# Optimization experiments

Hardware: AMD Instinct MI355X
Metric: run time of the kernel (lower is better)

The kernel has to match this reference:

```python
import jax, jax.numpy as jnp
import numpy as np

D_MODEL = 768
D_STATE = 16
D_CONV = 4
EXPAND = 2
HEADDIM = 64
D_INNER = EXPAND * D_MODEL          # 1536
NHEADS = D_INNER // HEADDIM         # 24
CONV_DIM = D_INNER + 2 * D_STATE    # 1568
D_IN_PROJ = 2 * D_INNER + 2 * D_STATE + NHEADS  # 3128
BATCH, SEQ = 4, 2048


def _mamba_params(key, scale=0.02):
    ks = jax.random.split(key, 5)
    return dict(
        in_w=jax.random.normal(ks[0], (D_MODEL, D_IN_PROJ), jnp.float32) * scale,
        conv_w=jax.random.normal(ks[1], (CONV_DIM, D_CONV), jnp.float32) * scale,
        conv_b=jnp.zeros((CONV_DIM,), jnp.float32),
        dt_bias=jax.random.normal(ks[2], (NHEADS,), jnp.float32) * 0.1,
        A_log=jnp.log(jax.random.uniform(ks[3], (NHEADS,), jnp.float32, 1.0, 16.0)),
        D=jnp.ones((NHEADS,), jnp.float32),
        norm_w=jnp.ones((D_INNER,), jnp.float32),
        out_w=jax.random.normal(ks[4], (D_INNER, D_MODEL), jnp.float32) * scale,
    )


def setup_inputs() -> dict:
    key = jax.random.key(0)
    kx, kf, kb, k1, k2 = jax.random.split(key, 5)
    f = _mamba_params(kf)
    b = _mamba_params(kb)
    k1a, k1b = jax.random.split(k1)
    inp = {
        'x': jax.random.normal(kx, (BATCH, SEQ, D_MODEL), jnp.float32),
        'ln1_w': jnp.ones((D_MODEL,), jnp.float32), 'ln1_b': jnp.zeros((D_MODEL,), jnp.float32),
        'ln2_w': jnp.ones((D_MODEL,), jnp.float32), 'ln2_b': jnp.zeros((D_MODEL,), jnp.float32),
        'ffn_w1': jax.random.normal(k1a, (2 * D_MODEL, 4 * D_MODEL), jnp.float32) * 0.02,
        'ffn_b1': jnp.zeros((4 * D_MODEL,), jnp.float32),
        'ffn_w2': jax.random.normal(k1b, (4 * D_MODEL, D_MODEL), jnp.float32) * 0.02,
        'ffn_b2': jnp.zeros((D_MODEL,), jnp.float32),
    }
    for name, p in (('f', f), ('b', b)):
        for k, v in p.items():
            inp[name + '_' + k] = v
    return inp


def _layernorm(x, w, b, eps=1e-5):
    m = jnp.mean(x, -1, keepdims=True)
    v = jnp.mean((x - m) ** 2, -1, keepdims=True)
    return (x - m) * jax.lax.rsqrt(v + eps) * w + b


def _mamba2(u, in_w, conv_w, conv_b, dt_bias, A_log, D, norm_w, out_w):
    b, l, _ = u.shape
    zxbcdt = u @ in_w                               # (b,l,d_in_proj)
    z = zxbcdt[..., :D_INNER]
    xBC = zxbcdt[..., D_INNER:D_INNER + CONV_DIM]
    dt = jax.nn.softplus(zxbcdt[..., -NHEADS:] + dt_bias)   # (b,l,h)
    # depthwise causal conv1d (kernel D_CONV) + SiLU
    xpad = jnp.pad(xBC, ((0, 0), (D_CONV - 1, 0), (0, 0)))
    xc = sum(conv_w[:, k] * xpad[:, k:k + l, :] for k in range(D_CONV)) + conv_b
    xc = jax.nn.silu(xc)
    xh = xc[..., :D_INNER].reshape(b, l, NHEADS, HEADDIM)
    Bm = xc[..., D_INNER:D_INNER + D_STATE]          # (b,l,n), ngroups=1
    Cm = xc[..., D_INNER + D_STATE:]                 # (b,l,n)
    A = -jnp.exp(A_log)                              # (h,)
    dA = jnp.exp(dt * A)                             # (b,l,h)

    def step(h, inp):
        dA_t, dt_t, B_t, C_t, x_t = inp              # (b,h),(b,h),(b,n),(b,n),(b,h,p)
        h = h * dA_t[:, :, None, None] + (dt_t[:, :, None] * x_t)[..., None] * B_t[:, None, None, :]
        y = jnp.einsum('bhpn,bn->bhp', h, C_t)
        return h, y

    h0 = jnp.zeros((b, NHEADS, HEADDIM, D_STATE), u.dtype)
    xs = (dA.transpose(1, 0, 2), dt.transpose(1, 0, 2), Bm.transpose(1, 0, 2),
          Cm.transpose(1, 0, 2), xh.transpose(1, 0, 2, 3))
    _, ys = jax.lax.scan(step, h0, xs)               # ys: (l,b,h,p)
    y = ys.transpose(1, 0, 2, 3) + D[None, None, :, None] * xh
    y = y.reshape(b, l, D_INNER)
    # gated RMSNorm: rmsnorm(y * silu(z)) * weight
    yz = y * jax.nn.silu(z)
    yz = yz * jax.lax.rsqrt(jnp.mean(yz * yz, -1, keepdims=True) + 1e-5) * norm_w
    return yz @ out_w


def reference(x, ln1_w, ln1_b, ln2_w, ln2_b,
              f_in_w, f_conv_w, f_conv_b, f_dt_bias, f_A_log, f_D, f_norm_w, f_out_w,
              b_in_w, b_conv_w, b_conv_b, b_dt_bias, b_A_log, b_D, b_norm_w, b_out_w,
              ffn_w1, ffn_b1, ffn_w2, ffn_b2):
    xn = _layernorm(x, ln1_w, ln1_b)
    fo = _mamba2(xn, f_in_w, f_conv_w, f_conv_b, f_dt_bias, f_A_log, f_D, f_norm_w, f_out_w)
    bo = _mamba2(jnp.flip(xn, 1), b_in_w, b_conv_w, b_conv_b, b_dt_bias, b_A_log, b_D, b_norm_w, b_out_w)
    bo = jnp.flip(bo, 1)
    bi = jnp.concatenate([fo, bo], -1)
    h = jax.nn.gelu(bi @ ffn_w1 + ffn_b1, approximate=False)
    h = jax.nn.gelu(h @ ffn_w2 + ffn_b2, approximate=False)
    # dropout is identity in eval mode
    return _layernorm(x + h, ln2_w, ln2_b)
```

## Files before the change

kernel.cpp:

```cpp
#include <hip/hip_runtime.h>
#include <math.h>

#define BATCH   4
#define SEQ     2048
#define DMODEL  768
#define DSTATE  16
#define DCONV   4
#define HEADDIM 64
#define DINNER  1536
#define NHEADS  24
#define CONVDIM 1568
#define DINPROJ 3128
#define DFFN    3072
#define ROWS    (BATCH*SEQ)
#define QCH     128
#define NCHUNK  (SEQ/QCH)

typedef __attribute__((ext_vector_type(8))) short bhalf8;
typedef __attribute__((ext_vector_type(4))) float floatx4;

__device__ __forceinline__ float gelu_f(float x) {
    return 0.5f * x * (1.0f + erff(x * 0.70710678118654752f));
}

__device__ __forceinline__ void splitRNE(float v, unsigned short& h, unsigned short& l) {
    unsigned u = __float_as_uint(v);
    unsigned rr = u + 0x7FFFu + ((u >> 16) & 1u);
    unsigned short hi = (unsigned short)(rr >> 16);
    float rem = v - __uint_as_float(((unsigned)hi) << 16);
    unsigned u2 = __float_as_uint(rem);
    unsigned r2 = u2 + 0x7FFFu + ((u2 >> 16) & 1u);
    h = hi;
    l = (unsigned short)(r2 >> 16);
}

__device__ __forceinline__ void gl16(const unsigned short* g, unsigned short* l) {
    __builtin_amdgcn_global_load_lds(
        (const __attribute__((address_space(1))) void*)g,
        (__attribute__((address_space(3))) void*)l, 16, 0, 0);
}

__device__ __forceinline__ float2 blockReduce2(float a, float b) {
    #pragma unroll
    for (int o = 32; o > 0; o >>= 1) {
        a += __shfl_down(a, o, 64);
        b += __shfl_down(b, o, 64);
    }
    __shared__ float sa[4], sb[4];
    int w = threadIdx.x >> 6, lane = threadIdx.x & 63;
    if (lane == 0) { sa[w] = a; sb[w] = b; }
    __syncthreads();
    if (threadIdx.x == 0) {
        int nw = blockDim.x >> 6;
        for (int i = 1; i < nw; ++i) { a += sa[i]; b += sb[i]; }
        sa[0] = a; sb[0] = b;
    }
    __syncthreads();
    return make_float2(sa[0], sb[0]);
}

__global__ __launch_bounds__(256) void ln_kernel(
    const float* __restrict__ x, const float* __restrict__ res,
    const float* __restrict__ w, const float* __restrict__ b,
    float* __restrict__ out)
{
    int r = blockIdx.x;
    const float* xr = x + (size_t)r * DMODEL;
    float v[3]; float s = 0.f, ss = 0.f;
    #pragma unroll
    for (int i = 0; i < 3; ++i) {
        int c = threadIdx.x + i * 256;
        float t = xr[c];
        if (res) t += res[(size_t)r * DMODEL + c];
        v[i] = t; s += t; ss += t * t;
    }
    float2 red = blockReduce2(s, ss);
    float mean = red.x * (1.0f / DMODEL);
    float var  = red.y * (1.0f / DMODEL) - mean * mean;
    float inv  = rsqrtf(var + 1e-5f);
    #pragma unroll
    for (int i = 0; i < 3; ++i) {
        int c = threadIdx.x + i * 256;
        out[(size_t)r * DMODEL + c] = (v[i] - mean) * inv * w[c] + b[c];
    }
}

__global__ __launch_bounds__(256) void ln_split_kernel(
    const float* __restrict__ x,
    const float* __restrict__ w, const float* __restrict__ b,
    unsigned short* __restrict__ H, unsigned short* __restrict__ L)
{
    int r = blockIdx.x;
    const float* xr = x + (size_t)r * DMODEL;
    float v[3]; float s = 0.f, ss = 0.f;
    #pragma unroll
    for (int i = 0; i < 3; ++i) {
        int c = threadIdx.x + i * 256;
        float t = xr[c];
        v[i] = t; s += t; ss += t * t;
    }
    float2 red = blockReduce2(s, ss);
    float mean = red.x * (1.0f / DMODEL);
    float var  = red.y * (1.0f / DMODEL) - mean * mean;
    float inv  = rsqrtf(var + 1e-5f);
    #pragma unroll
    for (int i = 0; i < 3; ++i) {
        int c = threadIdx.x + i * 256;
        float o = (v[i] - mean) * inv * w[c] + b[c];
        unsigned short h, l;
        splitRNE(o, h, l);
        H[(size_t)r * DMODEL + c] = h;
        L[(size_t)r * DMODEL + c] = l;
    }
}

__global__ __launch_bounds__(256) void wconv(
    const float* __restrict__ W, unsigned short* __restrict__ TH,
    unsigned short* __restrict__ TL, int K, int N)
{
    __shared__ float t[32][33];
    int tx = threadIdx.x & 31, ty = threadIdx.x >> 5;
    int kb = blockIdx.y * 32, nb = blockIdx.x * 32;
    #pragma unroll
    for (int i = 0; i < 4; ++i) {
        int k = kb + ty + i * 8, n = nb + tx;
        t[ty + i * 8][tx] = (k < K && n < N) ? W[(size_t)k * N + n] : 0.f;
    }
    __syncthreads();
    #pragma unroll
    for (int i = 0; i < 4; ++i) {
        int n = nb + ty + i * 8, k = kb + tx;
        if (n < N && k < K) {
            unsigned short hi, lo;
            splitRNE(t[tx][ty + i * 8], hi, lo);
            TH[(size_t)n * K + k] = hi;
            TL[(size_t)n * K + k] = lo;
        }
    }
}

__global__ __launch_bounds__(256) void gemm3(
    const unsigned short* __restrict__ AHg, const unsigned short* __restrict__ ALg,
    const unsigned short* __restrict__ BHg, const unsigned short* __restrict__ BLg,
    float* __restrict__ C, unsigned short* __restrict__ CHo, unsigned short* __restrict__ CLo,
    const float* __restrict__ bias,
    int M, int N, int K, int ldc, int coloff,
    int revA, int revC, int act)
{
    (void)M;
    __shared__ __align__(16) unsigned short AsH[128 * 32], AsL[128 * 32];
    __shared__ __align__(16) unsigned short BsH[128 * 32], BsL[128 * 32];

    const int tid = threadIdx.x;
    const int m0 = blockIdx.y * 128;
    const int n0 = blockIdx.x * 128;

    size_t aoff[2], boff[2];
    int lofs[2];
    #pragma unroll
    for (int q = 0; q < 2; ++q) {
        int row = (tid >> 2) + 64 * q;
        int sd  = (tid & 3) ^ ((row >> 1) & 3);
        int ar = m0 + row;
        if (revA) ar = (ar & ~(SEQ - 1)) + (SEQ - 1 - (ar & (SEQ - 1)));
        aoff[q] = (size_t)ar * K + sd * 8;
        boff[q] = (size_t)(n0 + row) * K + sd * 8;
        lofs[q] = (tid + 256 * q) * 8;
    }

    auto stage = [&](int k0) {
        #pragma unroll
        for (int q = 0; q < 2; ++q) {
            gl16(AHg + aoff[q] + k0, AsH + lofs[q]);
            gl16(ALg + aoff[q] + k0, AsL + lofs[q]);
            gl16(BHg + boff[q] + k0, BsH + lofs[q]);
            gl16(BLg + boff[q] + k0, BsL + lofs[q]);
        }
    };

    auto frag = [&](const unsigned short* buf, int row, int slot) -> bhalf8 {
        int sp = slot ^ ((row >> 1) & 3);
        return *(const bhalf8*)(buf + row * 32 + sp * 8);
    };

    const int w = tid >> 6, lane = tid & 63;
    const int rw = (w >> 1) * 64, cw = (w & 1) * 64;
    const int lr = lane & 15;
    const int lq = lane >> 4;

    floatx4 acc[4][4];
    const floatx4 fz = {0.f, 0.f, 0.f, 0.f};
    #pragma unroll
    for (int i = 0; i < 4; ++i)
        #pragma unroll
        for (int j = 0; j < 4; ++j) acc[i][j] = fz;

    const int ktiles = K >> 5;
    stage(0);
    for (int kt = 0; kt < ktiles; ++kt) {
        __syncthreads();
        bhalf8 ah[4], al[4], bh[4], bl[4];
        #pragma unroll
        for (int i = 0; i < 4; ++i) {
            int ra = rw + i * 16 + lr;
            int rb = cw + i * 16 + lr;
            ah[i] = frag(AsH, ra, lq);
            al[i] = frag(AsL, ra, lq);
            bh[i] = frag(BsH, rb, lq);
            bl[i] = frag(BsL, rb, lq);
        }
        __syncthreads();
        if (kt + 1 < ktiles) stage((kt + 1) * 32);
        #pragma unroll
        for (int i = 0; i < 4; ++i)
            #pragma unroll
            for (int j = 0; j < 4; ++j) {
                acc[i][j] = __builtin_amdgcn_mfma_f32_16x16x32_bf16(ah[i], bh[j], acc[i][j], 0, 0, 0);
                acc[i][j] = __builtin_amdgcn_mfma_f32_16x16x32_bf16(ah[i], bl[j], acc[i][j], 0, 0, 0);
                acc[i][j] = __builtin_amdgcn_mfma_f32_16x16x32_bf16(al[i], bh[j], acc[i][j], 0, 0, 0);
            }
    }

    #pragma unroll
    for (int i = 0; i < 4; ++i) {
        #pragma unroll
        for (int j = 0; j < 4; ++j) {
            int gc = n0 + cw + j * 16 + lr;
            if (gc < N) {
                float bv = bias ? bias[gc] : 0.f;
                #pragma unroll
                for (int rg = 0; rg < 4; ++rg) {
                    int gm = m0 + rw + i * 16 + lq * 4 + rg;
                    if (revC) gm = (gm & ~(SEQ - 1)) + (SEQ - 1 - (gm & (SEQ - 1)));
                    float v = acc[i][j][rg] + bv;
                    if (act) v = gelu_f(v);
                    size_t o = (size_t)gm * ldc + coloff + gc;
                    if (CHo) {
                        unsigned short h, l;
                        splitRNE(v, h, l);
                        CHo[o] = h; CLo[o] = l;
                    } else {
                        C[o] = v;
                    }
                }
            }
        }
    }
}

__global__ __launch_bounds__(256) void conv_kernel(
    const float* __restrict__ zx, const float* __restrict__ cw,
    const float* __restrict__ cb, float* __restrict__ xcv,
    float* __restrict__ bc)
{
    int c = blockIdx.x * 256 + threadIdx.x;
    int r = blockIdx.y;
    if (c >= CONVDIM) return;
    int t = r & (SEQ - 1);
    int rb = r & ~(SEQ - 1);
    float acc = cb[c];
    #pragma unroll
    for (int k = 0; k < DCONV; ++k) {
        int tt = t - (DCONV - 1) + k;
        if (tt >= 0)
            acc += cw[c * DCONV + k] * zx[(size_t)(rb + tt) * DINPROJ + DINNER + c];
    }
    float v = acc / (1.0f + expf(-acc));
    if (c < DINNER) xcv[(size_t)r * DINNER + c] = v;
    else            bc[(size_t)r * 32 + (c - DINNER)] = v;
}

__global__ __launch_bounds__(256) void dt_kernel(
    const float* __restrict__ zx, const float* __restrict__ dt_bias,
    const float* __restrict__ A_log, float* __restrict__ dtda)
{
    int i = blockIdx.x * 256 + threadIdx.x;
    if (i >= ROWS * NHEADS) return;
    int r = i / NHEADS, h = i - r * NHEADS;
    float v = zx[(size_t)r * DINPROJ + (DINPROJ - NHEADS) + h] + dt_bias[h];
    float dt = (v > 20.f) ? v : log1pf(expf(v));
    float A = -expf(A_log[h]);
    dtda[(size_t)r * 48 + h] = dt;
    dtda[(size_t)r * 48 + 24 + h] = expf(dt * A);
}

__global__ __launch_bounds__(64) void scan_a(
    const float* __restrict__ xcv, const float* __restrict__ bc,
    const float* __restrict__ dtda, const float* __restrict__ Dp,
    float* __restrict__ yout, float* __restrict__ S, float* __restrict__ cd)
{
    int blk = blockIdx.x;
    int bh = blk / NCHUNK, c = blk - bh * NCHUNK;
    int b = bh / NHEADS, h = bh - b * NHEADS;
    int p = threadIdx.x;
    float hs[DSTATE] = {};
    float Dv = Dp[h];
    float cum = 1.f;
    int t0 = c * QCH;
    for (int t = t0; t < t0 + QCH; ++t) {
        size_t r = (size_t)b * SEQ + t;
        float dt = dtda[r * 48 + h];
        float dA = dtda[r * 48 + 24 + h];
        float x  = xcv[r * DINNER + h * HEADDIM + p];
        cum *= dA;
        float coef = dt * x;
        const float* bcr = bc + r * 32;
        float y = 0.f;
        #pragma unroll
        for (int n = 0; n < DSTATE; ++n) {
            hs[n] = hs[n] * dA + coef * bcr[n];
            y += hs[n] * bcr[16 + n];
        }
        yout[r * DINPROJ + DINNER + h * HEADDIM + p] = y + Dv * x;
        if (p == 0) cd[r * NHEADS + h] = cum;
    }
    float* Sp = S + (((size_t)bh * NCHUNK + c) * HEADDIM + p) * DSTATE;
    #pragma unroll
    for (int n = 0; n < DSTATE; ++n) Sp[n] = hs[n];
}

__global__ __launch_bounds__(64) void scan_b(
    const float* __restrict__ cd, float* __restrict__ S)
{
    int bh = blockIdx.x;
    int b = bh / NHEADS, h = bh - b * NHEADS;
    int p = threadIdx.x;
    float H[DSTATE] = {};
    for (int c = 0; c < NCHUNK; ++c) {
        float* Sp = S + (((size_t)bh * NCHUNK + c) * HEADDIM + p) * DSTATE;
        float P = cd[((size_t)b * SEQ + c * QCH + QCH - 1) * NHEADS + h];
        float s[DSTATE];
        #pragma unroll
        for (int n = 0; n < DSTATE; ++n) s[n] = Sp[n];
        #pragma unroll
        for (int n = 0; n < DSTATE; ++n) Sp[n] = H[n];
        #pragma unroll
        for (int n = 0; n < DSTATE; ++n) H[n] = P * H[n] + s[n];
    }
}

__global__ __launch_bounds__(64) void scan_c(
    const float* __restrict__ bc, const float* __restrict__ cd,
    const float* __restrict__ S, float* __restrict__ yout)
{
    int blk = blockIdx.x;
    int bh = blk / (NCHUNK - 1), c = blk - bh * (NCHUNK - 1) + 1;
    int b = bh / NHEADS, h = bh - b * NHEADS;
    int p = threadIdx.x;
    const float* Hp = S + (((size_t)bh * NCHUNK + c) * HEADDIM + p) * DSTATE;
    float H[DSTATE];
    #pragma unroll
    for (int n = 0; n < DSTATE; ++n) H[n] = Hp[n];
    int t0 = c * QCH;
    for (int t = t0; t < t0 + QCH; ++t) {
        size_t r = (size_t)b * SEQ + t;
        const float* Cr = bc + r * 32 + 16;
        float dot = 0.f;
        #pragma unroll
        for (int n = 0; n < DSTATE; ++n) dot += H[n] * Cr[n];
        float cum = cd[r * NHEADS + h];
        yout[r * DINPROJ + DINNER + h * HEADDIM + p] += cum * dot;
    }
}

__global__ __launch_bounds__(256) void gnorm_kernel(
    const float* __restrict__ zx, const float* __restrict__ nw,
    unsigned short* __restrict__ H, unsigned short* __restrict__ L)
{
    int r = blockIdx.x;
    const float* zr = zx + (size_t)r * DINPROJ;
    float v[6]; float ss = 0.f;
    #pragma unroll
    for (int i = 0; i < 6; ++i) {
        int c = threadIdx.x + i * 256;
        float z = zr[c];
        float y = zr[DINNER + c];
        float t = y * z / (1.0f + expf(-z));
        v[i] = t; ss += t * t;
    }
    float2 red = blockReduce2(ss, 0.f);
    float sc = rsqrtf(red.x * (1.0f / DINNER) + 1e-5f);
    #pragma unroll
    for (int i = 0; i < 6; ++i) {
        int c = threadIdx.x + i * 256;
        float o = v[i] * sc * nw[c];
        unsigned short h, l;
        splitRNE(o, h, l);
        H[(size_t)r * DINNER + c] = h;
        L[(size_t)r * DINNER + c] = l;
    }
}

extern "C" void kernel_launch(void* const* d_in, const int* in_sizes, int n_in,
                              void* d_out, int out_size, void* d_ws, size_t ws_size,
                              hipStream_t stream)
{
    (void)in_sizes; (void)n_in; (void)out_size; (void)ws_size;
    const float* x     = (const float*)d_in[0];
    const float* ln1w  = (const float*)d_in[1];
    const float* ln1b  = (const float*)d_in[2];
    const float* ln2w  = (const float*)d_in[3];
    const float* ln2b  = (const float*)d_in[4];
    const float* ffnw1 = (const float*)d_in[5];
    const float* ffnb1 = (const float*)d_in[6];
    const float* ffnw2 = (const float*)d_in[7];
    const float* ffnb2 = (const float*)d_in[8];
    const float* p[2][8];
    for (int d = 0; d < 2; ++d)
        for (int i = 0; i < 8; ++i)
            p[d][i] = (const float*)d_in[9 + d * 8 + i];

    float* ws   = (float*)d_ws;
    float* zx   = ws;
    float* bi   = zx + (size_t)ROWS * DINPROJ;
    float* S    = bi + (size_t)ROWS * DINNER;
    float* Wbuf = S  + (size_t)ROWS * DINNER;
    float* bcb  = Wbuf + 2402304;
    float* dtda = bcb + (size_t)ROWS * 32;
    float* Sbuf = Wbuf;
    float* cdbf = Wbuf + (size_t)BATCH * NHEADS * NCHUNK * HEADDIM * DSTATE;

    unsigned short* xnH = (unsigned short*)d_out;
    unsigned short* xnL = xnH + (size_t)ROWS * DMODEL;
    float* xcv = S;
    unsigned short* znH = (unsigned short*)S;
    unsigned short* znL = znH + (size_t)ROWS * DINNER;
    unsigned short* biH = (unsigned short*)bi;
    unsigned short* biL = biH + (size_t)ROWS * DINNER;
    unsigned short* hmH = (unsigned short*)zx;
    unsigned short* hmL = hmH + (size_t)ROWS * DFFN;
    float* ffo = S + 4718592;

    ln_split_kernel<<<ROWS, 256, 0, stream>>>(x, ln1w, ln1b, xnH, xnL);

    for (int d = 0; d < 2; ++d) {
        unsigned short* WH = (unsigned short*)Wbuf;
        unsigned short* WL = WH + (size_t)DINPROJ * DMODEL;
        wconv<<<dim3((DINPROJ + 31) / 32, DMODEL / 32), 256, 0, stream>>>(
            p[d][0], WH, WL, DMODEL, DINPROJ);
        gemm3<<<dim3((DINPROJ + 127) / 128, ROWS / 128), 256, 0, stream>>>(
            xnH, xnL, WH, WL, zx, nullptr, nullptr, nullptr,
            ROWS, DINPROJ, DMODEL, DINPROJ, 0, d, 0, 0);
        conv_kernel<<<dim3(7, ROWS), 256, 0, stream>>>(zx, p[d][1], p[d][2], xcv, bcb);
        dt_kernel<<<(ROWS * NHEADS + 255) / 256, 256, 0, stream>>>(
            zx, p[d][3], p[d][4], dtda);
        scan_a<<<BATCH * NHEADS * NCHUNK, 64, 0, stream>>>(
            xcv, bcb, dtda, p[d][5], zx, Sbuf, cdbf);
        scan_b<<<BATCH * NHEADS, 64, 0, stream>>>(cdbf, Sbuf);
        scan_c<<<BATCH * NHEADS * (NCHUNK - 1), 64, 0, stream>>>(
            bcb, cdbf, Sbuf, zx);
        gnorm_kernel<<<ROWS, 256, 0, stream>>>(zx, p[d][6], znH, znL);
        unsigned short* WL2 = WH + (size_t)DMODEL * DINNER;
        wconv<<<dim3(DMODEL / 32, DINNER / 32), 256, 0, stream>>>(
            p[d][7], WH, WL2, DINNER, DMODEL);
        gemm3<<<dim3(DMODEL / 128, ROWS / 128), 256, 0, stream>>>(
            znH, znL, WH, WL2, nullptr, biH, biL, nullptr,
            ROWS, DMODEL, DINNER, DINNER, d * DMODEL, 0, d, 0);
    }

    {
        unsigned short* WH = (unsigned short*)S;
        unsigned short* WL = WH + (size_t)DFFN * DINNER;
        wconv<<<dim3(DFFN / 32, DINNER / 32), 256, 0, stream>>>(
            ffnw1, WH, WL, DINNER, DFFN);
        gemm3<<<dim3(DFFN / 128, ROWS / 128), 256, 0, stream>>>(
            biH, biL, WH, WL, nullptr, hmH, hmL, ffnb1,
            ROWS, DFFN, DINNER, DFFN, 0, 0, 0, 1);
    }
    {
        unsigned short* WH = (unsigned short*)S;
        unsigned short* WL = WH + (size_t)DMODEL * DFFN;
        wconv<<<dim3(DMODEL / 32, DFFN / 32), 256, 0, stream>>>(
            ffnw2, WH, WL, DFFN, DMODEL);
        gemm3<<<dim3(DMODEL / 128, ROWS / 128), 256, 0, stream>>>(
            hmH, hmL, WH, WL, ffo, nullptr, nullptr, ffnb2,
            ROWS, DMODEL, DFFN, DMODEL, 0, 0, 0, 1);
    }
    ln_kernel<<<ROWS, 256, 0, stream>>>(x, ffo, ln2w, ln2b, (float*)d_out);
}
```

Measured before the change: 1.461 ms.

## Add 256x256-tile double-buffered bf16x3 GEMM for in_proj and FFN1

Adds a new GEMM kernel with 256x256 output tiles, 512 threads, double-buffered async global-to-LDS loads, an XOR swizzle against bank conflicts, XCD-aware block remapping and setprio around the MFMA bursts. It replaces the 128x128 gemm3 for the two in-projection GEMMs and the first FFN GEMM, aiming for more data reuse per tile and overlap of loads with MFMA work. Larger tiles lower the block count (about 416 or 384 blocks), risk wasted work on the ragged N=3128 edge, and may run at low occupancy. B rows beyond N are loaded without bounds checks for the 3128-wide case.

```diff
diff --git a/kernel.cpp b/kernel.cpp
--- a/kernel.cpp
+++ b/kernel.cpp
@@ -38,6 +38,12 @@
     __builtin_amdgcn_global_load_lds(
         (const __attribute__((address_space(1))) void*)g,
         (__attribute__((address_space(3))) void*)l, 16, 0, 0);
+}
+
+__device__ __forceinline__ void bar() {
+    asm volatile("" ::: "memory");
+    __builtin_amdgcn_s_barrier();
+    asm volatile("" ::: "memory");
 }
 
 __device__ __forceinline__ float2 blockReduce2(float a, float b) {
@@ -248,6 +254,143 @@
     }
 }
 
+__global__ __launch_bounds__(512, 1) void gemm8(
+    const unsigned short* __restrict__ AHg, const unsigned short* __restrict__ ALg,
+    const unsigned short* __restrict__ BHg, const unsigned short* __restrict__ BLg,
+    float* __restrict__ C, unsigned short* __restrict__ CHo, unsigned short* __restrict__ CLo,
+    const float* __restrict__ bias,
+    int M, int N, int K, int ldc, int coloff,
+    int revA, int revC, int act)
+{
+    (void)M;
+    __shared__ __align__(16) unsigned short AsH[2][256 * 32], AsL[2][256 * 32];
+    __shared__ __align__(16) unsigned short BsH[2][256 * 32], BsL[2][256 * 32];
+
+    const int tid = threadIdx.x;
+
+    const int gx = gridDim.x;
+    int lin = blockIdx.y * gx + blockIdx.x;
+    const int nwg = gx * gridDim.y;
+    if ((nwg & 7) == 0) lin = (lin & 7) * (nwg >> 3) + (lin >> 3);
+    const int m0 = (lin / gx) * 256;
+    const int n0 = (lin % gx) * 256;
+
+    size_t aoff[2], boff[2];
+    int lofs[2];
+    #pragma unroll
+    for (int q = 0; q < 2; ++q) {
+        int row = (tid >> 2) + 128 * q;
+        int sd  = (tid & 3) ^ ((row >> 1) & 3);
+        int ar = m0 + row;
+        if (revA) ar = (ar & ~(SEQ - 1)) + (SEQ - 1 - (ar & (SEQ - 1)));
+        aoff[q] = (size_t)ar * K + sd * 8;
+        boff[q] = (size_t)(n0 + row) * K + sd * 8;
+        lofs[q] = (tid + 512 * q) * 8;
+    }
+
+    auto stage = [&](int k0, int b) {
+        #pragma unroll
+        for (int q = 0; q < 2; ++q) {
+            gl16(AHg + aoff[q] + k0, &AsH[b][lofs[q]]);
+            gl16(ALg + aoff[q] + k0, &AsL[b][lofs[q]]);
+            gl16(BHg + boff[q] + k0, &BsH[b][lofs[q]]);
+            gl16(BLg + boff[q] + k0, &BsL[b][lofs[q]]);
+        }
+    };
+
+    const int wid = tid >> 6, lane = tid & 63;
+    const int wrb = (wid >> 2) * 128;
+    const int wcb = (wid & 3) * 64;
+    const int lr = lane & 15;
+    const int lq = lane >> 4;
+
+    auto frag = [&](const unsigned short* buf, int row) -> bhalf8 {
+        int sp = lq ^ ((row >> 1) & 3);
+        return *(const bhalf8*)(buf + row * 32 + sp * 8);
+    };
+
+    floatx4 acc[8][4];
+    const floatx4 fz = {0.f, 0.f, 0.f, 0.f};
+    #pragma unroll
+    for (int i = 0; i < 8; ++i)
+        #pragma unroll
+        for (int j = 0; j < 4; ++j) acc[i][j] = fz;
+
+    const int ktiles = K >> 5;
+
+    stage(0, 0);
+    for (int kt = 0; kt < ktiles; ++kt) {
+        const int cb = kt & 1;
+        if (kt + 1 < ktiles) {
+            stage((kt + 1) * 32, cb ^ 1);
+            asm volatile("s_waitcnt vmcnt(8)" ::: "memory");
+        } else {
+            asm volatile("s_waitcnt vmcnt(0)" ::: "memory");
+        }
+        bar();
+
+        const unsigned short* pAH = AsH[cb];
+        const unsigned short* pAL = AsL[cb];
+        const unsigned short* pBH = BsH[cb];
+        const unsigned short* pBL = BsL[cb];
+
+        bhalf8 bh[4], bl[4];
+        #pragma unroll
+        for (int j = 0; j < 4; ++j) {
+            int rb2 = wcb + j * 16 + lr;
+            bh[j] = frag(pBH, rb2);
+            bl[j] = frag(pBL, rb2);
+        }
+
+        #pragma unroll
+        for (int p = 0; p < 4; ++p) {
+            const int i0 = 2 * p, i1 = 2 * p + 1;
+            int r0 = wrb + i0 * 16 + lr;
+            int r1 = wrb + i1 * 16 + lr;
+            bhalf8 ah0 = frag(pAH, r0), al0 = frag(pAL, r0);
+            bhalf8 ah1 = frag(pAH, r1), al1 = frag(pAL, r1);
+            __builtin_amdgcn_s_setprio(1);
+            #pragma unroll
+            for (int j = 0; j < 4; ++j) {
+                acc[i0][j] = __builtin_amdgcn_mfma_f32_16x16x32_bf16(ah0, bh[j], acc[i0][j], 0, 0, 0);
+                acc[i0][j] = __builtin_amdgcn_mfma_f32_16x16x32_bf16(ah0, bl[j], acc[i0][j], 0, 0, 0);
+                acc[i0][j] = __builtin_amdgcn_mfma_f32_16x16x32_bf16(al0, bh[j], acc[i0][j], 0, 0, 0);
+                acc[i1][j] = __builtin_amdgcn_mfma_f32_16x16x32_bf16(ah1, bh[j], acc[i1][j], 0, 0, 0);
+                acc[i1][j] = __builtin_amdgcn_mfma_f32_16x16x32_bf16(ah1, bl[j], acc[i1][j], 0, 0, 0);
+                acc[i1][j] = __builtin_amdgcn_mfma_f32_16x16x32_bf16(al1, bh[j], acc[i1][j], 0, 0, 0);
+            }
+            __builtin_amdgcn_s_setprio(0);
+            bar();
+        }
+    }
+
+    #pragma unroll
+    for (int i = 0; i < 8; ++i) {
+        #pragma unroll
+        for (int j = 0; j < 4; ++j) {
+            int gc = n0 + wcb + j * 16 + lr;
+            if (gc < N) {
+                float bv = bias ? bias[gc] : 0.f;
+                #pragma unroll
+                for (int rg = 0; rg < 4; ++rg) {
+                    int gm = m0 + wrb + i * 16 + lq * 4 + rg;
+                    if (revC) gm = (gm & ~(SEQ - 1)) + (SEQ - 1 - (gm & (SEQ - 1)));
+                    float v = acc[i][j][rg] + bv;
+                    if (act) v = gelu_f(v);
+                    size_t o = (size_t)gm * ldc + coloff + gc;
+                    if (CHo) {
+                        unsigned short h, l;
+                        splitRNE(v, h, l);
+                        CHo[o] = h; CLo[o] = l;
+                    } else {
+                        C[o] = v;
+                    }
+                }
+            }
+        }
+    }
+}
+
 __global__ __launch_bounds__(256) void conv_kernel(
     const float* __restrict__ zx, const float* __restrict__ cw,
     const float* __restrict__ cb, float* __restrict__ xcv,
@@ -438,7 +581,7 @@
         unsigned short* WL = WH + (size_t)DINPROJ * DMODEL;
         wconv<<<dim3((DINPROJ + 31) / 32, DMODEL / 32), 256, 0, stream>>>(
             p[d][0], WH, WL, DMODEL, DINPROJ);
-        gemm3<<<dim3((DINPROJ + 127) / 128, ROWS / 128), 256, 0, stream>>>(
+        gemm8<<<dim3((DINPROJ + 255) / 256, ROWS / 256), 512, 0, stream>>>(
             xnH, xnL, WH, WL, zx, nullptr, nullptr, nullptr,
             ROWS, DINPROJ, DMODEL, DINPROJ, 0, d, 0, 0);
         conv_kernel<<<dim3(7, ROWS), 256, 0, stream>>>(zx, p[d][1], p[d][2], xcv, bcb);
@@ -463,7 +606,7 @@
         unsigned short* WL = WH + (size_t)DFFN * DINNER;
         wconv<<<dim3(DFFN / 32, DINNER / 32), 256, 0, stream>>>(
             ffnw1, WH, WL, DINNER, DFFN);
-        gemm3<<<dim3(DFFN / 128, ROWS / 128), 256, 0, stream>>>(
+        gemm8<<<dim3(DFFN / 256, ROWS / 256), 512, 0, stream>>>(
             biH, biL, WH, WL, nullptr, hmH, hmL, ffnb1,
             ROWS, DFFN, DINNER, DFFN, 0, 0, 0, 1);
     }
```

Measured after the change: 1.583 ms. 1.08x slower.

## Double-buffer GEMM LDS tiles, vectorize conv kernel, interleave dt/dA layout

Applied to the files above, without the earlier changes.

The split-bf16 GEMM now keeps two LDS buffers per operand. The next K-tile's global-to-LDS loads are issued before the MFMAs on the current tile, and each iteration ends with a single waitcnt plus barrier instead of two __syncthreads. MFMA issue priority is raised during the compute phase. Separately, the depthwise conv kernel handles four channels per thread with float4 loads and stores, and dt/dA are stored interleaved as float2 so the scan reads them in one load. The GEMM change doubles LDS per block to 64KB, which may lower occupancy.

```diff
diff --git a/kernel.cpp b/kernel.cpp
--- a/kernel.cpp
+++ b/kernel.cpp
@@ -40,6 +40,12 @@
         (__attribute__((address_space(3))) void*)l, 16, 0, 0);
 }
 
+__device__ __forceinline__ void bar() {
+    asm volatile("" ::: "memory");
+    __builtin_amdgcn_s_barrier();
+    asm volatile("" ::: "memory");
+}
+
 __device__ __forceinline__ float2 blockReduce2(float a, float b) {
     #pragma unroll
     for (int o = 32; o > 0; o >>= 1) {
@@ -148,8 +154,8 @@
     int revA, int revC, int act)
 {
     (void)M;
-    __shared__ __align__(16) unsigned short AsH[128 * 32], AsL[128 * 32];
-    __shared__ __align__(16) unsigned short BsH[128 * 32], BsL[128 * 32];
+    __shared__ __align__(16) unsigned short AsH[2][128 * 32], AsL[2][128 * 32];
+    __shared__ __align__(16) unsigned short BsH[2][128 * 32], BsL[2][128 * 32];
 
     const int tid = threadIdx.x;
     const int m0 = blockIdx.y * 128;
@@ -168,13 +174,13 @@
         lofs[q] = (tid + 256 * q) * 8;
     }
 
-    auto stage = [&](int k0) {
+    auto stage = [&](int k0, int b) {
         #pragma unroll
         for (int q = 0; q < 2; ++q) {
-            gl16(AHg + aoff[q] + k0, AsH + lofs[q]);
-            gl16(ALg + aoff[q] + k0, AsL + lofs[q]);
-            gl16(BHg + boff[q] + k0, BsH + lofs[q]);
-            gl16(BLg + boff[q] + k0, BsL + lofs[q]);
+            gl16(AHg + aoff[q] + k0, &AsH[b][lofs[q]]);
+            gl16(ALg + aoff[q] + k0, &AsL[b][lofs[q]]);
+            gl16(BHg + boff[q] + k0, &BsH[b][lofs[q]]);
+            gl16(BLg + boff[q] + k0, &BsL[b][lofs[q]]);
         }
     };
 
@@ -196,21 +202,30 @@
         for (int j = 0; j < 4; ++j) acc[i][j] = fz;
 
     const int ktiles = K >> 5;
-    stage(0);
+    stage(0, 0);
+    asm volatile("s_waitcnt vmcnt(0)" ::: "memory");
+    bar();
+
     for (int kt = 0; kt < ktiles; ++kt) {
-        __syncthreads();
+        const int cb = kt & 1;
+        if (kt + 1 < ktiles) stage((kt + 1) * 32, cb ^ 1);
+
+        const unsigned short* pAH = AsH[cb];
+        const unsigned short* pAL = AsL[cb];
+        const unsigned short* pBH = BsH[cb];
+        const unsigned short* pBL = BsL[cb];
         bhalf8 ah[4], al[4], bh[4], bl[4];
         #pragma unroll
         for (int i = 0; i < 4; ++i) {
             int ra = rw + i * 16 + lr;
             int rb = cw + i * 16 + lr;
-            ah[i] = frag(AsH, ra, lq);
-            al[i] = frag(AsL, ra, lq);
-            bh[i] = frag(BsH, rb, lq);
-            bl[i] = frag(BsL, rb, lq);
+            ah[i] = frag(pAH, ra, lq);
+            al[i] = frag(pAL, ra, lq);
+            bh[i] = frag(pBH, rb, lq);
+            bl[i] = frag(pBL, rb, lq);
         }
-        __syncthreads();
-        if (kt + 1 < ktiles) stage((kt + 1) * 32);
+
+        __builtin_amdgcn_s_setprio(1);
         #pragma unroll
         for (int i = 0; i < 4; ++i)
             #pragma unroll
@@ -219,6 +234,10 @@
                 acc[i][j] = __builtin_amdgcn_mfma_f32_16x16x32_bf16(ah[i], bl[j], acc[i][j], 0, 0, 0);
                 acc[i][j] = __builtin_amdgcn_mfma_f32_16x16x32_bf16(al[i], bh[j], acc[i][j], 0, 0, 0);
             }
+        __builtin_amdgcn_s_setprio(0);
+
+        asm volatile("s_waitcnt vmcnt(0)" ::: "memory");
+        bar();
     }
 
     #pragma unroll
@@ -253,21 +272,31 @@
     const float* __restrict__ cb, float* __restrict__ xcv,
     float* __restrict__ bc)
 {
-    int c = blockIdx.x * 256 + threadIdx.x;
+    int cg = blockIdx.x * 256 + threadIdx.x;
+    if (cg >= CONVDIM / 4) return;
+    int c = cg * 4;
     int r = blockIdx.y;
-    if (c >= CONVDIM) return;
     int t = r & (SEQ - 1);
     int rb = r & ~(SEQ - 1);
-    float acc = cb[c];
+    float4 acc = *(const float4*)&cb[c];
     #pragma unroll
     for (int k = 0; k < DCONV; ++k) {
         int tt = t - (DCONV - 1) + k;
-        if (tt >= 0)
-            acc += cw[c * DCONV + k] * zx[(size_t)(rb + tt) * DINPROJ + DINNER + c];
-    }
-    float v = acc / (1.0f + expf(-acc));
-    if (c < DINNER) xcv[(size_t)r * DINNER + c] = v;
-    else            bc[(size_t)r * 32 + (c - DINNER)] = v;
+        if (tt >= 0) {
+            float4 xv = *(const float4*)&zx[(size_t)(rb + tt) * DINPROJ + DINNER + c];
+            acc.x += cw[(c + 0) * DCONV + k] * xv.x;
+            acc.y += cw[(c + 1) * DCONV + k] * xv.y;
+            acc.z += cw[(c + 2) * DCONV + k] * xv.z;
+            acc.w += cw[(c + 3) * DCONV + k] * xv.w;
+        }
+    }
+    float4 v;
+    v.x = acc.x / (1.0f + expf(-acc.x));
+    v.y = acc.y / (1.0f + expf(-acc.y));
+    v.z = acc.z / (1.0f + expf(-acc.z));
+    v.w = acc.w / (1.0f + expf(-acc.w));
+    if (c < DINNER) *(float4*)&xcv[(size_t)r * DINNER + c] = v;
+    else            *(float4*)&bc[(size_t)r * 32 + (c - DINNER)] = v;
 }
 
 __global__ __launch_bounds__(256) void dt_kernel(
@@ -280,8 +309,8 @@
     float v = zx[(size_t)r * DINPROJ + (DINPROJ - NHEADS) + h] + dt_bias[h];
     float dt = (v > 20.f) ? v : log1pf(expf(v));
     float A = -expf(A_log[h]);
-    dtda[(size_t)r * 48 + h] = dt;
-    dtda[(size_t)r * 48 + 24 + h] = expf(dt * A);
+    float2 o = make_float2(dt, expf(dt * A));
+    *(float2*)&dtda[(size_t)r * 48 + 2 * h] = o;
 }
 
 __global__ __launch_bounds__(64) void scan_a(
@@ -299,8 +328,9 @@
     int t0 = c * QCH;
     for (int t = t0; t < t0 + QCH; ++t) {
         size_t r = (size_t)b * SEQ + t;
-        float dt = dtda[r * 48 + h];
-        float dA = dtda[r * 48 + 24 + h];
+        float2 dd = *(const float2*)&dtda[r * 48 + 2 * h];
+        float dt = dd.x;
+        float dA = dd.y;
         float x  = xcv[r * DINNER + h * HEADDIM + p];
         cum *= dA;
         float coef = dt * x;
@@ -441,7 +471,7 @@
         gemm3<<<dim3((DINPROJ + 127) / 128, ROWS / 128), 256, 0, stream>>>(
             xnH, xnL, WH, WL, zx, nullptr, nullptr, nullptr,
             ROWS, DINPROJ, DMODEL, DINPROJ, 0, d, 0, 0);
-        conv_kernel<<<dim3(7, ROWS), 256, 0, stream>>>(zx, p[d][1], p[d][2], xcv, bcb);
+        conv_kernel<<<dim3(2, ROWS), 256, 0, stream>>>(zx, p[d][1], p[d][2], xcv, bcb);
         dt_kernel<<<(ROWS * NHEADS + 255) / 256, 256, 0, stream>>>(
             zx, p[d][3], p[d][4], dtda);
         scan_a<<<BATCH * NHEADS * NCHUNK, 64, 0, stream>>>(
```

Result: slower. 1.625 ms (+11.3%).
